# Performance work log

Measured on AMD Instinct MI355X. Metric: run time of the kernel, lower is better.

## Reference

```python
import jax, jax.numpy as jnp
import numpy as np

N_NODES = 50000
N_EDGES = 800000
IN_C, HID_C, OUT_C = 128, 128, 64


def setup_inputs() -> dict:
    key = jax.random.key(0)
    ks = jax.random.split(key, 8)
    x = jax.random.normal(ks[0], (N_NODES, IN_C), dtype=jnp.float32)
    edge_index = jax.random.randint(ks[1], (2, N_EDGES), 0, N_NODES, dtype=jnp.int64)
    def glorot(k, shape):
        lim = np.sqrt(6.0 / (shape[0] + shape[1])).astype(np.float32)
        return jax.random.uniform(k, shape, jnp.float32, -lim, lim)
    return {
        "x": x,
        "edge_index": edge_index,
        "W1l": glorot(ks[2], (IN_C, HID_C)),
        "b1": jnp.zeros((HID_C,), jnp.float32),
        "W1r": glorot(ks[3], (IN_C, HID_C)),
        "W2l": glorot(ks[4], (HID_C, OUT_C)),
        "b2": jnp.zeros((OUT_C,), jnp.float32),
        "W2r": glorot(ks[5], (HID_C, OUT_C)),
    }


def _sage_conv(h, src, dst, Wl, bl, Wr):
    # mean aggregation over incoming edges (source -> target)
    n = h.shape[0]
    msg_sum = jax.ops.segment_sum(h[src], dst, num_segments=n)          # [N, d]
    deg = jax.ops.segment_sum(jnp.ones((src.shape[0],), h.dtype), dst, num_segments=n)
    agg = msg_sum / jnp.maximum(deg, 1.0)[:, None]                      # zero-degree -> 0
    # lin_l(agg) + lin_r(h); lin_l carries the bias (PyG SAGEConv default)
    return agg @ Wl + bl + h @ Wr


def reference(x, edge_index, W1l, b1, W1r, W2l, b2, W2r):
    src, dst = edge_index[0], edge_index[1]
    h = jax.nn.relu(_sage_conv(x, src, dst, W1l, b1, W1r))
    # eval-mode forward: dropout is identity
    out = _sage_conv(h, src, dst, W2l, b2, W2r)
    return out
```

## Files before the change

kernel.cpp:

```cpp
#include <hip/hip_runtime.h>

#define N_NODES 50000
#define N_EDGES 800000
#define IN_C    128
#define HID_C   128
#define OUT_C   64
#define NQ      784
#define QBCAP   1536
#define QCAP    1536
#define EPB     2048
#define EBLKS   ((N_EDGES + EPB - 1) / EPB)
#define PACK_BLKS 192
#define MM1_BLKS  ((N_NODES + 63) / 64)
#define L2F_BLKS  NQ
#define HS_STRIDE 136

typedef unsigned short ushort_t;
typedef unsigned int   uint_t;
typedef unsigned char  uchar_t;
typedef __attribute__((ext_vector_type(8))) short bf16x8;
typedef __attribute__((ext_vector_type(4))) float f32x4;
typedef __attribute__((ext_vector_type(2))) float f32x2;

__device__ inline ushort_t f2bf(float f) {
    uint_t u = __float_as_uint(f);
    uint_t r = (u + 0x7fffu + ((u >> 16) & 1u)) >> 16;
    return (ushort_t)r;
}
__device__ inline float bflo(uint_t v) { return __uint_as_float(v << 16); }
__device__ inline float bfhi(uint_t v) { return __uint_as_float(v & 0xffff0000u); }
__device__ inline uchar_t f2fp8(float v) {
    return (uchar_t)(__builtin_amdgcn_cvt_pk_fp8_f32(v, v, 0, false) & 0xff);
}
__device__ inline void acc_fp8x4(float* a, uint_t d) {
    const f32x2 lo = __builtin_amdgcn_cvt_pk_f32_fp8((int)d, false);
    const f32x2 hi = __builtin_amdgcn_cvt_pk_f32_fp8((int)d, true);
    a[0] += lo.x; a[1] += lo.y; a[2] += hi.x; a[3] += hi.y;
}
__device__ inline void acc_uint4(float* a, const uint4 v) {
    acc_fp8x4(a + 0,  v.x);
    acc_fp8x4(a + 4,  v.y);
    acc_fp8x4(a + 8,  v.z);
    acc_fp8x4(a + 12, v.w);
}

__device__ inline void pack_one(const float* W, ushort_t* Wp, int K, int N, int idx) {
    const int j  = idx & 7;
    const int L  = (idx >> 3) & 63;
    const int t  = idx >> 9;
    const int KT = K / 32;
    const int kt = t % KT;
    const int ct = t / KT;
    const int k  = kt * 32 + (L >> 4) * 8 + j;
    const int n  = ct * 16 + (L & 15);
    Wp[idx] = f2bf(W[k * N + n]);
}

__global__ __launch_bounds__(256) void k0_kernel(
    const float* __restrict__ W1l, const float* __restrict__ W1r,
    const float* __restrict__ W2l, const float* __restrict__ W2r,
    ushort_t* __restrict__ wpack, int* __restrict__ gcur)
{
    const int b = blockIdx.x;
    if (b < PACK_BLKS) {
        const int tid = b * 256 + threadIdx.x;
        if (tid < 16384)      pack_one(W1l, wpack,          IN_C,  HID_C, tid);
        else if (tid < 32768) pack_one(W1r, wpack + 16384,  IN_C,  HID_C, tid - 16384);
        else if (tid < 40960) pack_one(W2l, wpack + 32768,  HID_C, OUT_C, tid - 32768);
        else if (tid < 49152) pack_one(W2r, wpack + 40960,  HID_C, OUT_C, tid - 40960);
    } else {
        for (int i = threadIdx.x; i < NQ; i += 256) gcur[i] = 0;
    }
}

__device__ inline void mm1_body(int bid, const float* __restrict__ x,
                                const ushort_t* __restrict__ wpack,
                                uchar_t* __restrict__ p1f, ushort_t* __restrict__ t1b)
{
    const int wave = threadIdx.x >> 6;
    const int lane = threadIdx.x & 63;
    const int quad = lane >> 4;
    const int m    = lane & 15;
    const int row0 = bid * 64 + wave * 16;
    const int arow = min(row0 + m, N_NODES - 1);

    const bf16x8* Bl = (const bf16x8*)(wpack);
    const bf16x8* Br = (const bf16x8*)(wpack + 16384);

    f32x4 accl[8], accr[8];
#pragma unroll
    for (int ct = 0; ct < 8; ++ct) { accl[ct] = (f32x4)(0.0f); accr[ct] = (f32x4)(0.0f); }

    const float* xbase = x + (size_t)arow * IN_C + quad * 8;
    float4 c0 = *(const float4*)(xbase);
    float4 c1 = *(const float4*)(xbase + 4);

#pragma unroll
    for (int kt = 0; kt < 4; ++kt) {
        float4 n0 = c0, n1 = c1;
        if (kt < 3) {
            n0 = *(const float4*)(xbase + (kt + 1) * 32);
            n1 = *(const float4*)(xbase + (kt + 1) * 32 + 4);
        }
        bf16x8 af;
        af[0] = (short)f2bf(c0.x); af[1] = (short)f2bf(c0.y);
        af[2] = (short)f2bf(c0.z); af[3] = (short)f2bf(c0.w);
        af[4] = (short)f2bf(c1.x); af[5] = (short)f2bf(c1.y);
        af[6] = (short)f2bf(c1.z); af[7] = (short)f2bf(c1.w);
#pragma unroll
        for (int ct = 0; ct < 8; ++ct) {
            const bf16x8 bl = Bl[(ct * 4 + kt) * 64 + lane];
            const bf16x8 br = Br[(ct * 4 + kt) * 64 + lane];
            accl[ct] = __builtin_amdgcn_mfma_f32_16x16x32_bf16(af, bl, accl[ct], 0, 0, 0);
            accr[ct] = __builtin_amdgcn_mfma_f32_16x16x32_bf16(af, br, accr[ct], 0, 0, 0);
        }
        c0 = n0; c1 = n1;
    }

#pragma unroll
    for (int r = 0; r < 4; ++r) {
        const int orow = row0 + quad * 4 + r;
        if (orow < N_NODES) {
#pragma unroll
            for (int ct = 0; ct < 8; ++ct) {
                const int col = ct * 16 + m;
                p1f[(size_t)orow * HID_C + col] = f2fp8(accl[ct][r]);
                t1b[(size_t)orow * HID_C + col] = f2bf(accr[ct][r]);
            }
        }
    }
}

__global__ __launch_bounds__(256) void k1_kernel(
    const float* __restrict__ x, const ushort_t* __restrict__ wpack,
    uchar_t* __restrict__ p1f, ushort_t* __restrict__ t1b,
    const int* __restrict__ src, const int* __restrict__ dst,
    int* gcur, int* __restrict__ ebuf)
{
    __shared__ int lh[NQ], gb2[NQ], lc[NQ];
    const int b = blockIdx.x;
    if (b < MM1_BLKS) {
        mm1_body(b, x, wpack, p1f, t1b);
        return;
    }
    const int blk = b - MM1_BLKS;
    const int t = threadIdx.x;
    for (int i = t; i < NQ; i += 256) lh[i] = 0;
    __syncthreads();
    const int e0 = blk * EPB + t * 8;
    int v8[8], b8[8];
    if (e0 < N_EDGES) {
        const int4 sa = *(const int4*)&src[e0];
        const int4 sb = *(const int4*)&src[e0 + 4];
        const int4 da = *(const int4*)&dst[e0];
        const int4 db = *(const int4*)&dst[e0 + 4];
        const int s8a[8] = {sa.x, sa.y, sa.z, sa.w, sb.x, sb.y, sb.z, sb.w};
        const int d8a[8] = {da.x, da.y, da.z, da.w, db.x, db.y, db.z, db.w};
#pragma unroll
        for (int j = 0; j < 8; ++j) {
            b8[j] = d8a[j] >> 6;
            v8[j] = (s8a[j] << 6) | (d8a[j] & 63);
            atomicAdd(&lh[b8[j]], 1);
        }
    } else {
#pragma unroll
        for (int j = 0; j < 8; ++j) b8[j] = -1;
    }
    __syncthreads();
    for (int i = t; i < NQ; i += 256) {
        const int run = lh[i];
        gb2[i] = (run > 0) ? atomicAdd(&gcur[i], run) : 0;
        lc[i] = 0;
    }
    __syncthreads();
#pragma unroll
    for (int j = 0; j < 8; ++j) {
        const int bk = b8[j];
        if (bk >= 0) {
            const int p   = atomicAdd(&lc[bk], 1);
            const int pos = gb2[bk] + p;
            if (pos < QBCAP) ebuf[bk * QBCAP + pos] = v8[j];
        }
    }
}

__global__ __launch_bounds__(256, 4) void l2f_kernel(
    const int* __restrict__ ebuf, const int* __restrict__ gcur,
    int* __restrict__ cnt, int* __restrict__ row_ptr, int* __restrict__ csr_g,
    const uchar_t* __restrict__ p1f, const ushort_t* __restrict__ t1b,
    const float* __restrict__ b1,
    const ushort_t* __restrict__ wpack,
    uchar_t* __restrict__ p2f, ushort_t* __restrict__ t2b)
{
    __shared__ ushort_t hs[64 * HS_STRIDE];
    __shared__ __align__(16) int csr_lds[QCAP];
    __shared__ int lh[64], lstart[64], lcur2[64];
    __shared__ int pool, ltotal;

    const int blk = blockIdx.x;
    const int tid = threadIdx.x;

    if (tid == 0) pool = 0;
    if (tid < 64) lh[tid] = 0;
    __syncthreads();

    const int nb   = min(gcur[blk], QBCAP);
    const int base = blk * QBCAP;
    int v0 = -1, v1 = -1, v2 = -1, v3 = -1, v4 = -1, v5 = -1;
    if (tid        < nb) v0 = ebuf[base + tid];
    if (tid + 256  < nb) v1 = ebuf[base + tid + 256];
    if (tid + 512  < nb) v2 = ebuf[base + tid + 512];
    if (tid + 768  < nb) v3 = ebuf[base + tid + 768];
    if (tid + 1024 < nb) v4 = ebuf[base + tid + 1024];
    if (tid + 1280 < nb) v5 = ebuf[base + tid + 1280];
    if (v0 >= 0) atomicAdd(&lh[v0 & 63], 1);
    if (v1 >= 0) atomicAdd(&lh[v1 & 63], 1);
    if (v2 >= 0) atomicAdd(&lh[v2 & 63], 1);
    if (v3 >= 0) atomicAdd(&lh[v3 & 63], 1);
    if (v4 >= 0) atomicAdd(&lh[v4 & 63], 1);
    if (v5 >= 0) atomicAdd(&lh[v5 & 63], 1);
    __syncthreads();
    if (tid < 64) {
        const int c = lh[tid];
        int v = c;
#pragma unroll
        for (int off = 1; off < 64; off <<= 1) {
            const int u = __shfl_up(v, off, 64);
            if (tid >= off) v += u;
        }
        const int ex = v - c;
        lstart[tid] = ex;
        lcur2[tid]  = ex;
        if (tid == 63) ltotal = v;
        const int node = blk * 64 + tid;
        if (node < N_NODES) { cnt[node] = c; row_ptr[node] = blk * QCAP + ex; }
    }
    __syncthreads();
    if (v0 >= 0) { const int p = atomicAdd(&lcur2[v0 & 63], 1); if (p < QCAP) csr_lds[p] = v0 >> 6; }
    if (v1 >= 0) { const int p = atomicAdd(&lcur2[v1 & 63], 1); if (p < QCAP) csr_lds[p] = v1 >> 6; }
    if (v2 >= 0) { const int p = atomicAdd(&lcur2[v2 & 63], 1); if (p < QCAP) csr_lds[p] = v2 >> 6; }
    if (v3 >= 0) { const int p = atomicAdd(&lcur2[v3 & 63], 1); if (p < QCAP) csr_lds[p] = v3 >> 6; }
    if (v4 >= 0) { const int p = atomicAdd(&lcur2[v4 & 63], 1); if (p < QCAP) csr_lds[p] = v4 >> 6; }
    if (v5 >= 0) { const int p = atomicAdd(&lcur2[v5 & 63], 1); if (p < QCAP) csr_lds[p] = v5 >> 6; }
    __syncthreads();
    {
        const int total = ltotal > QCAP ? QCAP : ltotal;
        const int nt4 = (total + 3) >> 2;
        int4* dst4 = (int4*)(csr_g + blk * QCAP);
        const int4* src4 = (const int4*)csr_lds;
        for (int i = tid; i < nt4; i += 256) dst4[i] = src4[i];
    }
    __syncthreads();

    const int c16 = tid & 7;
    const int gb  = (tid & 63) & 56;
    const uint4* p1v = (const uint4*)p1f;

    while (true) {
        int nl = 0;
        if (c16 == 0) nl = atomicAdd(&pool, 1);
        nl = __shfl(nl, gb, 64);
        if (nl >= 64) break;
        const int node = blk * 64 + nl;
        uint4 oL = make_uint4(0u, 0u, 0u, 0u);
        uint4 oH = make_uint4(0u, 0u, 0u, 0u);
        if (node < N_NODES) {
            const int start = lstart[nl];
            const int degi  = lh[nl];
            const size_t ib = (size_t)node * HID_C + c16 * 16;
            const uint4 tvL = *(const uint4*)(t1b + ib);
            const uint4 tvH = *(const uint4*)(t1b + ib + 8);
            float a[16];
#pragma unroll
            for (int z = 0; z < 16; ++z) a[z] = 0.0f;
            int e = 0;
            for (; e + 7 < degi; e += 8) {
                const int s0 = csr_lds[start + e + 0];
                const int s1 = csr_lds[start + e + 1];
                const int s2 = csr_lds[start + e + 2];
                const int s3 = csr_lds[start + e + 3];
                const int s4 = csr_lds[start + e + 4];
                const int s5 = csr_lds[start + e + 5];
                const int s6 = csr_lds[start + e + 6];
                const int s7 = csr_lds[start + e + 7];
                const uint4 w0 = p1v[(size_t)s0 * 8 + c16];
                const uint4 w1 = p1v[(size_t)s1 * 8 + c16];
                const uint4 w2 = p1v[(size_t)s2 * 8 + c16];
                const uint4 w3 = p1v[(size_t)s3 * 8 + c16];
                const uint4 w4 = p1v[(size_t)s4 * 8 + c16];
                const uint4 w5 = p1v[(size_t)s5 * 8 + c16];
                const uint4 w6 = p1v[(size_t)s6 * 8 + c16];
                const uint4 w7 = p1v[(size_t)s7 * 8 + c16];
                acc_uint4(a, w0); acc_uint4(a, w1); acc_uint4(a, w2); acc_uint4(a, w3);
                acc_uint4(a, w4); acc_uint4(a, w5); acc_uint4(a, w6); acc_uint4(a, w7);
            }
            for (; e + 3 < degi; e += 4) {
                const int s0 = csr_lds[start + e + 0];
                const int s1 = csr_lds[start + e + 1];
                const int s2 = csr_lds[start + e + 2];
                const int s3 = csr_lds[start + e + 3];
                const uint4 w0 = p1v[(size_t)s0 * 8 + c16];
                const uint4 w1 = p1v[(size_t)s1 * 8 + c16];
                const uint4 w2 = p1v[(size_t)s2 * 8 + c16];
                const uint4 w3 = p1v[(size_t)s3 * 8 + c16];
                acc_uint4(a, w0); acc_uint4(a, w1); acc_uint4(a, w2); acc_uint4(a, w3);
            }
            for (; e < degi; ++e) {
                const uint4 v = p1v[(size_t)csr_lds[start + e] * 8 + c16];
                acc_uint4(a, v);
            }
            const float inv = 1.0f / fmaxf((float)degi, 1.0f);
            float r[16];
#pragma unroll
            for (int z = 0; z < 4; ++z) {
                const float4 bv = *(const float4*)(b1 + c16 * 16 + z * 4);
                r[z*4+0] = bv.x; r[z*4+1] = bv.y; r[z*4+2] = bv.z; r[z*4+3] = bv.w;
            }
            const uint_t tw[8] = {tvL.x, tvL.y, tvL.z, tvL.w, tvH.x, tvH.y, tvH.z, tvH.w};
#pragma unroll
            for (int z = 0; z < 8; ++z) {
                r[z*2+0] = fmaxf(fmaf(a[z*2+0], inv, r[z*2+0] + bflo(tw[z])), 0.0f);
                r[z*2+1] = fmaxf(fmaf(a[z*2+1], inv, r[z*2+1] + bfhi(tw[z])), 0.0f);
            }
            oL.x = (uint_t)f2bf(r[0])  | ((uint_t)f2bf(r[1])  << 16);
            oL.y = (uint_t)f2bf(r[2])  | ((uint_t)f2bf(r[3])  << 16);
            oL.z = (uint_t)f2bf(r[4])  | ((uint_t)f2bf(r[5])  << 16);
            oL.w = (uint_t)f2bf(r[6])  | ((uint_t)f2bf(r[7])  << 16);
            oH.x = (uint_t)f2bf(r[8])  | ((uint_t)f2bf(r[9])  << 16);
            oH.y = (uint_t)f2bf(r[10]) | ((uint_t)f2bf(r[11]) << 16);
            oH.z = (uint_t)f2bf(r[12]) | ((uint_t)f2bf(r[13]) << 16);
            oH.w = (uint_t)f2bf(r[14]) | ((uint_t)f2bf(r[15]) << 16);
        }
        *(uint4*)&hs[nl * HS_STRIDE + c16 * 16] = oL;
        *(uint4*)&hs[nl * HS_STRIDE + c16 * 16 + 8] = oH;
    }
    __syncthreads();

    const int wv   = tid >> 6;
    const int lane = tid & 63;
    const int quad = lane >> 4;
    const int m    = lane & 15;
    const int row0 = blk * 64 + wv * 16;

    const bf16x8* Bl = (const bf16x8*)(wpack + 32768);
    const bf16x8* Br = (const bf16x8*)(wpack + 40960);

    f32x4 accl[4], accr[4];
#pragma unroll
    for (int ct = 0; ct < 4; ++ct) { accl[ct] = (f32x4)(0.0f); accr[ct] = (f32x4)(0.0f); }

#pragma unroll
    for (int kt = 0; kt < 4; ++kt) {
        const bf16x8 af = *(const bf16x8*)&hs[(wv * 16 + m) * HS_STRIDE + kt * 32 + quad * 8];
#pragma unroll
        for (int ct = 0; ct < 4; ++ct) {
            const bf16x8 bl = Bl[(ct * 4 + kt) * 64 + lane];
            const bf16x8 br = Br[(ct * 4 + kt) * 64 + lane];
            accl[ct] = __builtin_amdgcn_mfma_f32_16x16x32_bf16(af, bl, accl[ct], 0, 0, 0);
            accr[ct] = __builtin_amdgcn_mfma_f32_16x16x32_bf16(af, br, accr[ct], 0, 0, 0);
        }
    }

#pragma unroll
    for (int r = 0; r < 4; ++r) {
        const int orow = row0 + quad * 4 + r;
        if (orow < N_NODES) {
#pragma unroll
            for (int ct = 0; ct < 4; ++ct) {
                const int col = ct * 16 + m;
                p2f[(size_t)orow * OUT_C + col] = f2fp8(accl[ct][r]);
                t2b[(size_t)orow * OUT_C + col] = f2bf(accr[ct][r]);
            }
        }
    }
}

__global__ __launch_bounds__(256) void agg2_kernel(
    const uchar_t* __restrict__ p2f, const ushort_t* __restrict__ t2b,
    const float* __restrict__ b2, const int* __restrict__ row_ptr,
    const int* __restrict__ cnt, const int* __restrict__ csr,
    float* __restrict__ out)
{
    const int c16 = threadIdx.x & 3;
    const int grp = threadIdx.x >> 2;
    const uint4* p2v = (const uint4*)p2f;

    const int node = blockIdx.x * 64 + grp;
    if (node >= N_NODES) return;
    const int start = row_ptr[node];
    const int degi  = cnt[node];
    const size_t i = (size_t)node * OUT_C + c16 * 16;
    const uint4 tvL = *(const uint4*)(t2b + i);
    const uint4 tvH = *(const uint4*)(t2b + i + 8);
    float a[16];
#pragma unroll
    for (int z = 0; z < 16; ++z) a[z] = 0.0f;
    int e = 0;
    for (; e + 7 < degi; e += 8) {
        const int s0 = csr[start + e + 0];
        const int s1 = csr[start + e + 1];
        const int s2 = csr[start + e + 2];
        const int s3 = csr[start + e + 3];
        const int s4 = csr[start + e + 4];
        const int s5 = csr[start + e + 5];
        const int s6 = csr[start + e + 6];
        const int s7 = csr[start + e + 7];
        const uint4 w0 = p2v[(size_t)s0 * 4 + c16];
        const uint4 w1 = p2v[(size_t)s1 * 4 + c16];
        const uint4 w2 = p2v[(size_t)s2 * 4 + c16];
        const uint4 w3 = p2v[(size_t)s3 * 4 + c16];
        const uint4 w4 = p2v[(size_t)s4 * 4 + c16];
        const uint4 w5 = p2v[(size_t)s5 * 4 + c16];
        const uint4 w6 = p2v[(size_t)s6 * 4 + c16];
        const uint4 w7 = p2v[(size_t)s7 * 4 + c16];
        acc_uint4(a, w0); acc_uint4(a, w1); acc_uint4(a, w2); acc_uint4(a, w3);
        acc_uint4(a, w4); acc_uint4(a, w5); acc_uint4(a, w6); acc_uint4(a, w7);
    }
    for (; e + 3 < degi; e += 4) {
        const int s0 = csr[start + e + 0];
        const int s1 = csr[start + e + 1];
        const int s2 = csr[start + e + 2];
        const int s3 = csr[start + e + 3];
        const uint4 w0 = p2v[(size_t)s0 * 4 + c16];
        const uint4 w1 = p2v[(size_t)s1 * 4 + c16];
        const uint4 w2 = p2v[(size_t)s2 * 4 + c16];
        const uint4 w3 = p2v[(size_t)s3 * 4 + c16];
        acc_uint4(a, w0); acc_uint4(a, w1); acc_uint4(a, w2); acc_uint4(a, w3);
    }
    for (; e < degi; ++e) {
        const uint4 v = p2v[(size_t)csr[start + e] * 4 + c16];
        acc_uint4(a, v);
    }

    const float inv = 1.0f / fmaxf((float)degi, 1.0f);
    const uint_t tw[8] = {tvL.x, tvL.y, tvL.z, tvL.w, tvH.x, tvH.y, tvH.z, tvH.w};
#pragma unroll
    for (int z = 0; z < 4; ++z) {
        const float4 bv = *(const float4*)(b2 + c16 * 16 + z * 4);
        float4 o;
        o.x = fmaf(a[z*4+0], inv, bv.x + bflo(tw[z*2+0]));
        o.y = fmaf(a[z*4+1], inv, bv.y + bfhi(tw[z*2+0]));
        o.z = fmaf(a[z*4+2], inv, bv.z + bflo(tw[z*2+1]));
        o.w = fmaf(a[z*4+3], inv, bv.w + bfhi(tw[z*2+1]));
        *(float4*)(out + i + z * 4) = o;
    }
}

extern "C" void kernel_launch(void* const* d_in, const int* in_sizes, int n_in,
                              void* d_out, int out_size, void* d_ws, size_t ws_size,
                              hipStream_t stream)
{
    const float* x   = (const float*)d_in[0];
    const int*   ei  = (const int*)d_in[1];
    const float* W1l = (const float*)d_in[2];
    const float* b1  = (const float*)d_in[3];
    const float* W1r = (const float*)d_in[4];
    const float* W2l = (const float*)d_in[5];
    const float* b2  = (const float*)d_in[6];
    const float* W2r = (const float*)d_in[7];
    float* out = (float*)d_out;

    const int* src = ei;
    const int* dst = ei + N_EDGES;

    const size_t NH = (size_t)N_NODES * HID_C;
    const size_t NO = (size_t)N_NODES * OUT_C;
    const size_t EB = (size_t)NQ * QBCAP;
    const size_t CB = (size_t)NQ * QCAP;

    char* ws = (char*)d_ws;
    ushort_t* t1b   = (ushort_t*)ws;                   ws += NH * sizeof(ushort_t);
    ushort_t* t2b   = (ushort_t*)ws;                   ws += NO * sizeof(ushort_t);
    ushort_t* wpack = (ushort_t*)ws;                   ws += 49152 * sizeof(ushort_t);
    int* ebuf    = (int*)ws;                           ws += EB * sizeof(int);
    int* csr     = (int*)ws;                           ws += CB * sizeof(int);
    int* cnt     = (int*)ws;                           ws += N_NODES * sizeof(int);
    int* row_ptr = (int*)ws;                           ws += N_NODES * sizeof(int);
    int* gcur    = (int*)ws;                           ws += NQ * sizeof(int);
    ws += (16 - ((size_t)(ws - (char*)d_ws) & 15)) & 15;
    uchar_t* p1f = (uchar_t*)ws;                       ws += NH * sizeof(uchar_t);
    uchar_t* p2f = (uchar_t*)ws;                       ws += NO * sizeof(uchar_t);

    const size_t need = (size_t)(ws - (char*)d_ws);
    if (ws_size < need) return;

    k0_kernel<<<PACK_BLKS + 1, 256, 0, stream>>>(W1l, W1r, W2l, W2r, wpack, gcur);
    k1_kernel<<<MM1_BLKS + EBLKS, 256, 0, stream>>>(
        x, wpack, p1f, t1b, src, dst, gcur, ebuf);
    l2f_kernel<<<L2F_BLKS, 256, 0, stream>>>(
        ebuf, gcur, cnt, row_ptr, csr, p1f, t1b, b1, wpack, p2f, t2b);
    agg2_kernel<<<MM1_BLKS, 256, 0, stream>>>(
        p2f, t2b, b2, row_ptr, cnt, csr, out);
}
```

Before: 175.2 us.

## Halve destination bin size to 32 nodes and split layer-2 MFMA across waves

Destination binning now uses 32-node bins (1563 bins, capacity 768) instead of 64-node bins, so the fused layer-1 aggregation and layer-2 transform kernel launches about twice as many blocks, each handling fewer nodes with less LDS. The layer-2 MFMA work is split so each wave covers 16 rows by 2 column tiles. The 8-way unrolled gather loops are removed from both aggregation loops. The aim is more parallelism and occupancy for the latency-bound gather, at the cost of more per-block overhead, a larger k1 LDS histogram, and less memory-level parallelism per thread.

```diff
diff --git a/kernel.cpp b/kernel.cpp
--- a/kernel.cpp
+++ b/kernel.cpp
@@ -5,14 +5,13 @@
 #define IN_C    128
 #define HID_C   128
 #define OUT_C   64
-#define NQ      784
-#define QBCAP   1536
-#define QCAP    1536
+#define NBIN    1563
+#define BCAP8   768
+#define QCAP8   768
 #define EPB     2048
 #define EBLKS   ((N_EDGES + EPB - 1) / EPB)
 #define PACK_BLKS 192
 #define MM1_BLKS  ((N_NODES + 63) / 64)
-#define L2F_BLKS  NQ
 #define HS_STRIDE 136
 
 typedef unsigned short ushort_t;
@@ -69,7 +68,7 @@
         else if (tid < 40960) pack_one(W2l, wpack + 32768,  HID_C, OUT_C, tid - 32768);
         else if (tid < 49152) pack_one(W2r, wpack + 40960,  HID_C, OUT_C, tid - 40960);
     } else {
-        for (int i = threadIdx.x; i < NQ; i += 256) gcur[i] = 0;
+        for (int i = threadIdx.x; i < NBIN; i += 256) gcur[i] = 0;
     }
 }
 
@@ -137,7 +136,7 @@
     const int* __restrict__ src, const int* __restrict__ dst,
     int* gcur, int* __restrict__ ebuf)
 {
-    __shared__ int lh[NQ], gb2[NQ], lc[NQ];
+    __shared__ int lh[NBIN], gb2[NBIN], lc[NBIN];
     const int b = blockIdx.x;
     if (b < MM1_BLKS) {
         mm1_body(b, x, wpack, p1f, t1b);
@@ -145,7 +144,7 @@
     }
     const int blk = b - MM1_BLKS;
     const int t = threadIdx.x;
-    for (int i = t; i < NQ; i += 256) lh[i] = 0;
+    for (int i = t; i < NBIN; i += 256) lh[i] = 0;
     __syncthreads();
     const int e0 = blk * EPB + t * 8;
     int v8[8], b8[8];
@@ -158,8 +157,8 @@
         const int d8a[8] = {da.x, da.y, da.z, da.w, db.x, db.y, db.z, db.w};
 #pragma unroll
         for (int j = 0; j < 8; ++j) {
-            b8[j] = d8a[j] >> 6;
-            v8[j] = (s8a[j] << 6) | (d8a[j] & 63);
+            b8[j] = d8a[j] >> 5;
+            v8[j] = (s8a[j] << 5) | (d8a[j] & 31);
             atomicAdd(&lh[b8[j]], 1);
         }
     } else {
@@ -167,7 +166,7 @@
         for (int j = 0; j < 8; ++j) b8[j] = -1;
     }
     __syncthreads();
-    for (int i = t; i < NQ; i += 256) {
+    for (int i = t; i < NBIN; i += 256) {
         const int run = lh[i];
         gb2[i] = (run > 0) ? atomicAdd(&gcur[i], run) : 0;
         lc[i] = 0;
@@ -179,7 +178,7 @@
         if (bk >= 0) {
             const int p   = atomicAdd(&lc[bk], 1);
             const int pos = gb2[bk] + p;
-            if (pos < QBCAP) ebuf[bk * QBCAP + pos] = v8[j];
+            if (pos < BCAP8) ebuf[bk * BCAP8 + pos] = v8[j];
         }
     }
 }
@@ -192,61 +191,52 @@
     const ushort_t* __restrict__ wpack,
     uchar_t* __restrict__ p2f, ushort_t* __restrict__ t2b)
 {
-    __shared__ ushort_t hs[64 * HS_STRIDE];
-    __shared__ __align__(16) int csr_lds[QCAP];
-    __shared__ int lh[64], lstart[64], lcur2[64];
+    __shared__ ushort_t hs[32 * HS_STRIDE];
+    __shared__ __align__(16) int csr_lds[QCAP8];
+    __shared__ int lh[32], lstart[32], lcur2[32];
     __shared__ int pool, ltotal;
 
     const int blk = blockIdx.x;
     const int tid = threadIdx.x;
 
     if (tid == 0) pool = 0;
-    if (tid < 64) lh[tid] = 0;
-    __syncthreads();
-
-    const int nb   = min(gcur[blk], QBCAP);
-    const int base = blk * QBCAP;
-    int v0 = -1, v1 = -1, v2 = -1, v3 = -1, v4 = -1, v5 = -1;
-    if (tid        < nb) v0 = ebuf[base + tid];
-    if (tid + 256  < nb) v1 = ebuf[base + tid + 256];
-    if (tid + 512  < nb) v2 = ebuf[base + tid + 512];
-    if (tid + 768  < nb) v3 = ebuf[base + tid + 768];
-    if (tid + 1024 < nb) v4 = ebuf[base + tid + 1024];
-    if (tid + 1280 < nb) v5 = ebuf[base + tid + 1280];
-    if (v0 >= 0) atomicAdd(&lh[v0 & 63], 1);
-    if (v1 >= 0) atomicAdd(&lh[v1 & 63], 1);
-    if (v2 >= 0) atomicAdd(&lh[v2 & 63], 1);
-    if (v3 >= 0) atomicAdd(&lh[v3 & 63], 1);
-    if (v4 >= 0) atomicAdd(&lh[v4 & 63], 1);
-    if (v5 >= 0) atomicAdd(&lh[v5 & 63], 1);
-    __syncthreads();
-    if (tid < 64) {
+    if (tid < 32) lh[tid] = 0;
+    __syncthreads();
+
+    const int nb   = min(gcur[blk], BCAP8);
+    const int base = blk * BCAP8;
+    int v0 = -1, v1 = -1, v2 = -1;
+    if (tid       < nb) v0 = ebuf[base + tid];
+    if (tid + 256 < nb) v1 = ebuf[base + tid + 256];
+    if (tid + 512 < nb) v2 = ebuf[base + tid + 512];
+    if (v0 >= 0) atomicAdd(&lh[v0 & 31], 1);
+    if (v1 >= 0) atomicAdd(&lh[v1 & 31], 1);
+    if (v2 >= 0) atomicAdd(&lh[v2 & 31], 1);
+    __syncthreads();
+    if (tid < 32) {
         const int c = lh[tid];
         int v = c;
 #pragma unroll
-        for (int off = 1; off < 64; off <<= 1) {
-            const int u = __shfl_up(v, off, 64);
+        for (int off = 1; off < 32; off <<= 1) {
+            const int u = __shfl_up(v, off, 32);
             if (tid >= off) v += u;
         }
         const int ex = v - c;
         lstart[tid] = ex;
         lcur2[tid]  = ex;
-        if (tid == 63) ltotal = v;
-        const int node = blk * 64 + tid;
-        if (node < N_NODES) { cnt[node] = c; row_ptr[node] = blk * QCAP + ex; }
-    }
-    __syncthreads();
-    if (v0 >= 0) { const int p = atomicAdd(&lcur2[v0 & 63], 1); if (p < QCAP) csr_lds[p] = v0 >> 6; }
-    if (v1 >= 0) { const int p = atomicAdd(&lcur2[v1 & 63], 1); if (p < QCAP) csr_lds[p] = v1 >> 6; }
-    if (v2 >= 0) { const int p = atomicAdd(&lcur2[v2 & 63], 1); if (p < QCAP) csr_lds[p] = v2 >> 6; }
-    if (v3 >= 0) { const int p = atomicAdd(&lcur2[v3 & 63], 1); if (p < QCAP) csr_lds[p] = v3 >> 6; }
-    if (v4 >= 0) { const int p = atomicAdd(&lcur2[v4 & 63], 1); if (p < QCAP) csr_lds[p] = v4 >> 6; }
-    if (v5 >= 0) { const int p = atomicAdd(&lcur2[v5 & 63], 1); if (p < QCAP) csr_lds[p] = v5 >> 6; }
+        if (tid == 31) ltotal = v;
+        const int node = blk * 32 + tid;
+        if (node < N_NODES) { cnt[node] = c; row_ptr[node] = blk * QCAP8 + ex; }
+    }
+    __syncthreads();
+    if (v0 >= 0) { const int p = atomicAdd(&lcur2[v0 & 31], 1); if (p < QCAP8) csr_lds[p] = v0 >> 5; }
+    if (v1 >= 0) { const int p = atomicAdd(&lcur2[v1 & 31], 1); if (p < QCAP8) csr_lds[p] = v1 >> 5; }
+    if (v2 >= 0) { const int p = atomicAdd(&lcur2[v2 & 31], 1); if (p < QCAP8) csr_lds[p] = v2 >> 5; }
     __syncthreads();
     {
-        const int total = ltotal > QCAP ? QCAP : ltotal;
+        const int total = ltotal > QCAP8 ? QCAP8 : ltotal;
         const int nt4 = (total + 3) >> 2;
-        int4* dst4 = (int4*)(csr_g + blk * QCAP);
+        int4* dst4 = (int4*)(csr_g + blk * QCAP8);
         const int4* src4 = (const int4*)csr_lds;
         for (int i = tid; i < nt4; i += 256) dst4[i] = src4[i];
     }
@@ -260,8 +250,8 @@
         int nl = 0;
         if (c16 == 0) nl = atomicAdd(&pool, 1);
         nl = __shfl(nl, gb, 64);
-        if (nl >= 64) break;
-        const int node = blk * 64 + nl;
+        if (nl >= 32) break;
+        const int node = blk * 32 + nl;
         uint4 oL = make_uint4(0u, 0u, 0u, 0u);
         uint4 oH = make_uint4(0u, 0u, 0u, 0u);
         if (node < N_NODES) {
@@ -274,26 +264,6 @@
 #pragma unroll
             for (int z = 0; z < 16; ++z) a[z] = 0.0f;
             int e = 0;
-            for (; e + 7 < degi; e += 8) {
-                const int s0 = csr_lds[start + e + 0];
-                const int s1 = csr_lds[start + e + 1];
-                const int s2 = csr_lds[start + e + 2];
-                const int s3 = csr_lds[start + e + 3];
-                const int s4 = csr_lds[start + e + 4];
-                const int s5 = csr_lds[start + e + 5];
-                const int s6 = csr_lds[start + e + 6];
-                const int s7 = csr_lds[start + e + 7];
-                const uint4 w0 = p1v[(size_t)s0 * 8 + c16];
-                const uint4 w1 = p1v[(size_t)s1 * 8 + c16];
-                const uint4 w2 = p1v[(size_t)s2 * 8 + c16];
-                const uint4 w3 = p1v[(size_t)s3 * 8 + c16];
-                const uint4 w4 = p1v[(size_t)s4 * 8 + c16];
-                const uint4 w5 = p1v[(size_t)s5 * 8 + c16];
-                const uint4 w6 = p1v[(size_t)s6 * 8 + c16];
-                const uint4 w7 = p1v[(size_t)s7 * 8 + c16];
-                acc_uint4(a, w0); acc_uint4(a, w1); acc_uint4(a, w2); acc_uint4(a, w3);
-                acc_uint4(a, w4); acc_uint4(a, w5); acc_uint4(a, w6); acc_uint4(a, w7);
-            }
             for (; e + 3 < degi; e += 4) {
                 const int s0 = csr_lds[start + e + 0];
                 const int s1 = csr_lds[start + e + 1];
@@ -336,28 +306,31 @@
     }
     __syncthreads();
 
-    const int wv   = tid >> 6;
-    const int lane = tid & 63;
-    const int quad = lane >> 4;
-    const int m    = lane & 15;
-    const int row0 = blk * 64 + wv * 16;
+    const int wv    = tid >> 6;
+    const int lane  = tid & 63;
+    const int quad  = lane >> 4;
+    const int m     = lane & 15;
+    const int rhalf = wv & 1;
+    const int chalf = (wv >> 1) * 2;
+    const int row0  = blk * 32 + rhalf * 16;
 
     const bf16x8* Bl = (const bf16x8*)(wpack + 32768);
     const bf16x8* Br = (const bf16x8*)(wpack + 40960);
 
-    f32x4 accl[4], accr[4];
-#pragma unroll
-    for (int ct = 0; ct < 4; ++ct) { accl[ct] = (f32x4)(0.0f); accr[ct] = (f32x4)(0.0f); }
+    f32x4 accl[2], accr[2];
+#pragma unroll
+    for (int c2 = 0; c2 < 2; ++c2) { accl[c2] = (f32x4)(0.0f); accr[c2] = (f32x4)(0.0f); }
 
 #pragma unroll
     for (int kt = 0; kt < 4; ++kt) {
-        const bf16x8 af = *(const bf16x8*)&hs[(wv * 16 + m) * HS_STRIDE + kt * 32 + quad * 8];
-#pragma unroll
-        for (int ct = 0; ct < 4; ++ct) {
+        const bf16x8 af = *(const bf16x8*)&hs[(rhalf * 16 + m) * HS_STRIDE + kt * 32 + quad * 8];
+#pragma unroll
+        for (int c2 = 0; c2 < 2; ++c2) {
+            const int ct = chalf + c2;
             const bf16x8 bl = Bl[(ct * 4 + kt) * 64 + lane];
             const bf16x8 br = Br[(ct * 4 + kt) * 64 + lane];
-            accl[ct] = __builtin_amdgcn_mfma_f32_16x16x32_bf16(af, bl, accl[ct], 0, 0, 0);
-            accr[ct] = __builtin_amdgcn_mfma_f32_16x16x32_bf16(af, br, accr[ct], 0, 0, 0);
+            accl[c2] = __builtin_amdgcn_mfma_f32_16x16x32_bf16(af, bl, accl[c2], 0, 0, 0);
+            accr[c2] = __builtin_amdgcn_mfma_f32_16x16x32_bf16(af, br, accr[c2], 0, 0, 0);
         }
     }
 
@@ -366,10 +339,10 @@
         const int orow = row0 + quad * 4 + r;
         if (orow < N_NODES) {
 #pragma unroll
-            for (int ct = 0; ct < 4; ++ct) {
-                const int col = ct * 16 + m;
-                p2f[(size_t)orow * OUT_C + col] = f2fp8(accl[ct][r]);
-                t2b[(size_t)orow * OUT_C + col] = f2bf(accr[ct][r]);
+            for (int c2 = 0; c2 < 2; ++c2) {
+                const int col = (chalf + c2) * 16 + m;
+                p2f[(size_t)orow * OUT_C + col] = f2fp8(accl[c2][r]);
+                t2b[(size_t)orow * OUT_C + col] = f2bf(accr[c2][r]);
             }
         }
     }
@@ -396,26 +369,6 @@
 #pragma unroll
     for (int z = 0; z < 16; ++z) a[z] = 0.0f;
     int e = 0;
-    for (; e + 7 < degi; e += 8) {
-        const int s0 = csr[start + e + 0];
-        const int s1 = csr[start + e + 1];
-        const int s2 = csr[start + e + 2];
-        const int s3 = csr[start + e + 3];
-        const int s4 = csr[start + e + 4];
-        const int s5 = csr[start + e + 5];
-        const int s6 = csr[start + e + 6];
-        const int s7 = csr[start + e + 7];
-        const uint4 w0 = p2v[(size_t)s0 * 4 + c16];
-        const uint4 w1 = p2v[(size_t)s1 * 4 + c16];
-        const uint4 w2 = p2v[(size_t)s2 * 4 + c16];
-        const uint4 w3 = p2v[(size_t)s3 * 4 + c16];
-        const uint4 w4 = p2v[(size_t)s4 * 4 + c16];
-        const uint4 w5 = p2v[(size_t)s5 * 4 + c16];
-        const uint4 w6 = p2v[(size_t)s6 * 4 + c16];
-        const uint4 w7 = p2v[(size_t)s7 * 4 + c16];
-        acc_uint4(a, w0); acc_uint4(a, w1); acc_uint4(a, w2); acc_uint4(a, w3);
-        acc_uint4(a, w4); acc_uint4(a, w5); acc_uint4(a, w6); acc_uint4(a, w7);
-    }
     for (; e + 3 < degi; e += 4) {
         const int s0 = csr[start + e + 0];
         const int s1 = csr[start + e + 1];
@@ -465,8 +418,8 @@
 
     const size_t NH = (size_t)N_NODES * HID_C;
     const size_t NO = (size_t)N_NODES * OUT_C;
-    const size_t EB = (size_t)NQ * QBCAP;
-    const size_t CB = (size_t)NQ * QCAP;
+    const size_t EB = (size_t)NBIN * BCAP8;
+    const size_t CB = (size_t)NBIN * QCAP8;
 
     char* ws = (char*)d_ws;
     ushort_t* t1b   = (ushort_t*)ws;                   ws += NH * sizeof(ushort_t);
@@ -476,7 +429,7 @@
     int* csr     = (int*)ws;                           ws += CB * sizeof(int);
     int* cnt     = (int*)ws;                           ws += N_NODES * sizeof(int);
     int* row_ptr = (int*)ws;                           ws += N_NODES * sizeof(int);
-    int* gcur    = (int*)ws;                           ws += NQ * sizeof(int);
+    int* gcur    = (int*)ws;                           ws += NBIN * sizeof(int);
     ws += (16 - ((size_t)(ws - (char*)d_ws) & 15)) & 15;
     uchar_t* p1f = (uchar_t*)ws;                       ws += NH * sizeof(uchar_t);
     uchar_t* p2f = (uchar_t*)ws;                       ws += NO * sizeof(uchar_t);
@@ -487,7 +440,7 @@
     k0_kernel<<<PACK_BLKS + 1, 256, 0, stream>>>(W1l, W1r, W2l, W2r, wpack, gcur);
     k1_kernel<<<MM1_BLKS + EBLKS, 256, 0, stream>>>(
         x, wpack, p1f, t1b, src, dst, gcur, ebuf);
-    l2f_kernel<<<L2F_BLKS, 256, 0, stream>>>(
+    l2f_kernel<<<NBIN, 256, 0, stream>>>(
         ebuf, gcur, cnt, row_ptr, csr, p1f, t1b, b1, wpack, p2f, t2b);
     agg2_kernel<<<MM1_BLKS, 256, 0, stream>>>(
         p2f, t2b, b2, row_ptr, cnt, csr, out);
```

New measurement: 157.8 us. -10.0%, faster.
